# Kernel tuning notes

Hardware: AMD Instinct MI355X
Metric: run time of the kernel (lower is better)

The kernel has to match this reference:

```python
import jax, jax.numpy as jnp
import numpy as np

N, F, H, O = 16384, 64, 128, 512

def setup_inputs() -> dict:
    key = jax.random.key(0)
    ks = jax.random.split(key, 5)
    # PyTorch Linear default init: U(-1/sqrt(fan_in), 1/sqrt(fan_in))
    lim1 = 1.0  # fan_in = 1 for Linear(1, H)
    lim2 = 1.0 / np.sqrt(H)
    x = jax.random.normal(ks[0], (N, F), dtype=jnp.float32)
    W1 = jax.random.uniform(ks[1], (F, H), minval=-lim1, maxval=lim1, dtype=jnp.float32)
    b1 = jax.random.uniform(ks[2], (F, H), minval=-lim1, maxval=lim1, dtype=jnp.float32)
    W2 = jax.random.uniform(ks[3], (F, H, O), minval=-lim2, maxval=lim2, dtype=jnp.float32)
    b2 = jax.random.uniform(ks[4], (F, O), minval=-lim2, maxval=lim2, dtype=jnp.float32)
    return {"x": x, "W1": W1, "b1": b1, "W2": W2, "b2": b2}

def reference(x, W1, b1, W2, b2):
    # Per-feature MLP: h_f = W2_f @ elu(x_f * w1_f + b1_f) + b2_f, summed over f.
    # pre: [N, F, H] = outer-product of each scalar feature with its W1 row
    pre = x[:, :, None] * W1[None, :, :] + b1[None, :, :]
    a = jax.nn.elu(pre)                                  # [N, F, H]
    h = jnp.einsum('nfh,fho->no', a, W2)                 # sum over f and h
    h = h + jnp.sum(b2, axis=0)[None, :]                 # biases summed over F
    return h / jnp.sqrt(jnp.float32(F))
```

## Files before the change

### kernel.cpp

```cpp
#include <hip/hip_runtime.h>
#include <cstdint>

#define NROWS 16384
#define FDIM 64
#define HDIM 128
#define ODIM 512
#define KDIM 8192

#define BM 64
#define BN 256
#define BK 64

typedef short bf16x8 __attribute__((ext_vector_type(8)));
typedef float f32x4 __attribute__((ext_vector_type(4)));
typedef uint32_t u32x4 __attribute__((ext_vector_type(4)));

__device__ __forceinline__ uint16_t rne_bf16(float f) {
  uint32_t u = __builtin_bit_cast(uint32_t, f);
  u += 0x7fffu + ((u >> 16) & 1u);
  return (uint16_t)(u >> 16);
}

__global__ void prep_w2t(const float* __restrict__ W2, uint16_t* __restrict__ W2T) {
  __shared__ float tile[64][65];
  const int k0 = blockIdx.x * 64;
  const int o0 = blockIdx.y * 64;
  const int tx = threadIdx.x;
  const int ty = threadIdx.y;
#pragma unroll
  for (int j = 0; j < 8; ++j)
    tile[ty + 8 * j][tx] = W2[(size_t)(k0 + ty + 8 * j) * ODIM + o0 + tx];
  __syncthreads();
#pragma unroll
  for (int j = 0; j < 8; ++j)
    W2T[(size_t)(o0 + ty + 8 * j) * KDIM + k0 + tx] = rne_bf16(tile[tx][ty + 8 * j]);
}

__global__ void prep_small(const float* __restrict__ W1, const float* __restrict__ b1,
                           const float* __restrict__ b2, uint16_t* __restrict__ w1bf,
                           uint16_t* __restrict__ b1bf, float* __restrict__ b2sum) {
  const int t = blockIdx.x * 256 + threadIdx.x;
  w1bf[t] = rne_bf16(W1[t]);
  b1bf[t] = rne_bf16(b1[t]);
  if (t < ODIM) {
    float s = 0.f;
#pragma unroll
    for (int f = 0; f < FDIM; ++f) s += b2[(size_t)f * ODIM + t];
    b2sum[t] = s;
  }
}

__global__ __launch_bounds__(256, 3) void mlp_gemm(
    const float* __restrict__ x, const uint16_t* __restrict__ w1bf,
    const uint16_t* __restrict__ b1bf, const uint16_t* __restrict__ W2T,
    const float* __restrict__ b2sum, float* __restrict__ out) {
  __shared__ __align__(16) uint16_t As[BM * BK];
  __shared__ __align__(16) uint16_t Bs[BN * BK];

  const int tid = threadIdx.x;
  const int bid = blockIdx.x;
  const int o0 = (bid & 1) * BN;
  const int m0 = (bid >> 1) * BM;

  const int wid = tid >> 6;
  const int lane = tid & 63;
  const int wn = wid * 64;
  const int q = lane >> 4;
  const int r = lane & 15;

  const int ar = tid >> 3;
  const int ac = tid & 7;
  const int brow = lane >> 3;
  const int bcg = (lane & 7) ^ brow;

  f32x4 acc[4][4];
#pragma unroll
  for (int i = 0; i < 4; ++i)
#pragma unroll
    for (int j = 0; j < 4; ++j) acc[i][j] = {0.f, 0.f, 0.f, 0.f};

  for (int f = 0; f < FDIM; ++f) {
    float xv[2];
#pragma unroll
    for (int i = 0; i < 2; ++i)
      xv[i] = x[(size_t)(m0 + i * 32 + ar) * FDIM + f];

#pragma unroll
    for (int half = 0; half < 2; ++half) {
      const int kk = f * 2 + half;
      __syncthreads();

#pragma unroll
      for (int j = 0; j < 8; ++j) {
        const int chunk = wid * 8 + j;
        const uint16_t* gp =
            W2T + (size_t)(o0 + chunk * 8 + brow) * KDIM + kk * BK + bcg * 8;
        uint16_t* lp = &Bs[chunk * 512];
        __builtin_amdgcn_global_load_lds(
            (const __attribute__((address_space(1))) uint32_t*)gp,
            (__attribute__((address_space(3))) uint32_t*)lp, 16, 0, 0);
      }

      const int hoff = half * 64 + ac * 8;
      u32x4 w1d = *(const u32x4*)(w1bf + f * HDIM + hoff);
      u32x4 b1d = *(const u32x4*)(b1bf + f * HDIM + hoff);
      float w1f[8], b1f[8];
#pragma unroll
      for (int p = 0; p < 4; ++p) {
        w1f[2 * p]     = __builtin_bit_cast(float, w1d[p] << 16);
        w1f[2 * p + 1] = __builtin_bit_cast(float, w1d[p] & 0xffff0000u);
        b1f[2 * p]     = __builtin_bit_cast(float, b1d[p] << 16);
        b1f[2 * p + 1] = __builtin_bit_cast(float, b1d[p] & 0xffff0000u);
      }
#pragma unroll
      for (int i = 0; i < 2; ++i) {
        const int m = i * 32 + ar;
        u32x4 ov;
#pragma unroll
        for (int p = 0; p < 4; ++p) {
          float plo = fmaf(xv[i], w1f[2 * p], b1f[2 * p]);
          float phi = fmaf(xv[i], w1f[2 * p + 1], b1f[2 * p + 1]);
          float elo = plo > 0.f ? plo : __expf(plo) - 1.f;
          float ehi = phi > 0.f ? phi : __expf(phi) - 1.f;
          ov[p] = __builtin_amdgcn_perm(__builtin_bit_cast(uint32_t, ehi),
                                        __builtin_bit_cast(uint32_t, elo),
                                        0x07060302u);
        }
        *(u32x4*)&As[m * BK + ((ac ^ (m & 7)) * 8)] = ov;
      }
      __syncthreads();

#pragma unroll
      for (int kc = 0; kc < 2; ++kc) {
        bf16x8 af[4], bfr[4];
        const int cg = kc * 4 + q;
#pragma unroll
        for (int mt = 0; mt < 4; ++mt) {
          const int row = mt * 16 + r;
          af[mt] = *(const bf16x8*)&As[row * BK + ((cg ^ (row & 7)) * 8)];
        }
#pragma unroll
        for (int nt = 0; nt < 4; ++nt) {
          const int row = wn + nt * 16 + r;
          bfr[nt] = *(const bf16x8*)&Bs[row * BK + ((cg ^ (row & 7)) * 8)];
        }
#pragma unroll
        for (int mt = 0; mt < 4; ++mt)
#pragma unroll
          for (int nt = 0; nt < 4; ++nt)
            acc[mt][nt] = __builtin_amdgcn_mfma_f32_16x16x32_bf16(
                af[mt], bfr[nt], acc[mt][nt], 0, 0, 0);
      }
    }
  }

  float bsv[4];
#pragma unroll
  for (int nt = 0; nt < 4; ++nt) bsv[nt] = b2sum[o0 + wn + nt * 16 + r];
#pragma unroll
  for (int mt = 0; mt < 4; ++mt)
#pragma unroll
    for (int nt = 0; nt < 4; ++nt)
#pragma unroll
      for (int v = 0; v < 4; ++v) {
        const int row = m0 + mt * 16 + q * 4 + v;
        const int col = o0 + wn + nt * 16 + r;
        out[(size_t)row * ODIM + col] = (acc[mt][nt][v] + bsv[nt]) * 0.125f;
      }
}

extern "C" void kernel_launch(void* const* d_in, const int* in_sizes, int n_in,
                              void* d_out, int out_size, void* d_ws, size_t ws_size,
                              hipStream_t stream) {
  const float* x  = (const float*)d_in[0];
  const float* W1 = (const float*)d_in[1];
  const float* b1 = (const float*)d_in[2];
  const float* W2 = (const float*)d_in[3];
  const float* b2 = (const float*)d_in[4];
  float* out = (float*)d_out;

  char* ws = (char*)d_ws;
  float*    b2sum = (float*)ws;
  uint16_t* w1bf  = (uint16_t*)(ws + 4096);
  uint16_t* b1bf  = (uint16_t*)(ws + 4096 + 16384);
  uint16_t* W2T   = (uint16_t*)(ws + 65536);

  prep_w2t<<<dim3(KDIM / 64, ODIM / 64), dim3(64, 8), 0, stream>>>(W2, W2T);
  prep_small<<<32, 256, 0, stream>>>(W1, b1, b2, w1bf, b1bf, b2sum);
  mlp_gemm<<<(NROWS / BM) * (ODIM / BN), 256, 0, stream>>>(x, w1bf, b1bf, W2T,
                                                           b2sum, out);
}
```

Measured before the change: 254.8 us.

## Double-buffer LDS, widen tile to full N, and stagger ELU generation across waves

Each block now covers all 512 output columns with 512 threads, so the ELU activation tile for a row block is computed once instead of once per N-half. A and B tiles are double-buffered in LDS with a single barrier per K-step, and the next step's W2 prefetch and A generation overlap the current step's MFMAs. Half the waves generate A before their MFMAs and half after, which spreads the exp/ALU work against matrix work. The cost is about 144KB of LDS per block, allowing only one block per CU. The grid also shrinks to 256 blocks, which lowers occupancy and increases per-block register pressure.

```diff
diff --git a/kernel.cpp b/kernel.cpp
--- a/kernel.cpp
+++ b/kernel.cpp
@@ -6,9 +6,10 @@
 #define HDIM 128
 #define ODIM 512
 #define KDIM 8192
+#define NSTEPS 128
 
 #define BM 64
-#define BN 256
+#define BN 512
 #define BK 64
 
 typedef short bf16x8 __attribute__((ext_vector_type(8)));
@@ -50,17 +51,15 @@
   }
 }
 
-__global__ __launch_bounds__(256, 3) void mlp_gemm(
+__global__ __launch_bounds__(512, 2) void mlp_gemm(
     const float* __restrict__ x, const uint16_t* __restrict__ w1bf,
     const uint16_t* __restrict__ b1bf, const uint16_t* __restrict__ W2T,
     const float* __restrict__ b2sum, float* __restrict__ out) {
-  __shared__ __align__(16) uint16_t As[BM * BK];
-  __shared__ __align__(16) uint16_t Bs[BN * BK];
+  __shared__ __align__(16) uint16_t As[2][BM * BK];
+  __shared__ __align__(16) uint16_t Bs[2][BN * BK];
 
   const int tid = threadIdx.x;
-  const int bid = blockIdx.x;
-  const int o0 = (bid & 1) * BN;
-  const int m0 = (bid >> 1) * BM;
+  const int m0 = blockIdx.x * BM;
 
   const int wid = tid >> 6;
   const int lane = tid & 63;
@@ -79,84 +78,91 @@
 #pragma unroll
     for (int j = 0; j < 4; ++j) acc[i][j] = {0.f, 0.f, 0.f, 0.f};
 
-  for (int f = 0; f < FDIM; ++f) {
-    float xv[2];
+  auto stageB = [&](int step, int buf) {
 #pragma unroll
-    for (int i = 0; i < 2; ++i)
-      xv[i] = x[(size_t)(m0 + i * 32 + ar) * FDIM + f];
+    for (int j = 0; j < 8; ++j) {
+      const int chunk = wid * 8 + j;
+      const uint16_t* gp =
+          W2T + (size_t)(chunk * 8 + brow) * KDIM + step * BK + bcg * 8;
+      uint16_t* lp = &Bs[buf][chunk * 512];
+      __builtin_amdgcn_global_load_lds(
+          (const __attribute__((address_space(1))) uint32_t*)gp,
+          (__attribute__((address_space(3))) uint32_t*)lp, 16, 0, 0);
+    }
+  };
 
+  auto genA = [&](int step, int buf) {
+    const int f = step >> 1;
+    const int half = step & 1;
+    const float xv = x[(size_t)(m0 + ar) * FDIM + f];
+    const int hoff = half * 64 + ac * 8;
+    u32x4 w1d = *(const u32x4*)(w1bf + f * HDIM + hoff);
+    u32x4 b1d = *(const u32x4*)(b1bf + f * HDIM + hoff);
+    u32x4 ov;
 #pragma unroll
-    for (int half = 0; half < 2; ++half) {
-      const int kk = f * 2 + half;
-      __syncthreads();
+    for (int p = 0; p < 4; ++p) {
+      float wlo = __builtin_bit_cast(float, w1d[p] << 16);
+      float whi = __builtin_bit_cast(float, w1d[p] & 0xffff0000u);
+      float blo = __builtin_bit_cast(float, b1d[p] << 16);
+      float bhi = __builtin_bit_cast(float, b1d[p] & 0xffff0000u);
+      float plo = fmaf(xv, wlo, blo);
+      float phi = fmaf(xv, whi, bhi);
+      float elo = plo > 0.f ? plo : __expf(plo) - 1.f;
+      float ehi = phi > 0.f ? phi : __expf(phi) - 1.f;
+      ov[p] = __builtin_amdgcn_perm(__builtin_bit_cast(uint32_t, ehi),
+                                    __builtin_bit_cast(uint32_t, elo),
+                                    0x07060302u);
+    }
+    *(u32x4*)&As[buf][ar * BK + ((ac ^ (ar & 7)) * 8)] = ov;
+  };
 
+  auto domfma = [&](int buf) {
 #pragma unroll
-      for (int j = 0; j < 8; ++j) {
-        const int chunk = wid * 8 + j;
-        const uint16_t* gp =
-            W2T + (size_t)(o0 + chunk * 8 + brow) * KDIM + kk * BK + bcg * 8;
-        uint16_t* lp = &Bs[chunk * 512];
-        __builtin_amdgcn_global_load_lds(
-            (const __attribute__((address_space(1))) uint32_t*)gp,
-            (__attribute__((address_space(3))) uint32_t*)lp, 16, 0, 0);
-      }
-
-      const int hoff = half * 64 + ac * 8;
-      u32x4 w1d = *(const u32x4*)(w1bf + f * HDIM + hoff);
-      u32x4 b1d = *(const u32x4*)(b1bf + f * HDIM + hoff);
-      float w1f[8], b1f[8];
+    for (int kc = 0; kc < 2; ++kc) {
+      bf16x8 af[4], bfr[4];
+      const int cg = kc * 4 + q;
 #pragma unroll
-      for (int p = 0; p < 4; ++p) {
-        w1f[2 * p]     = __builtin_bit_cast(float, w1d[p] << 16);
-        w1f[2 * p + 1] = __builtin_bit_cast(float, w1d[p] & 0xffff0000u);
-        b1f[2 * p]     = __builtin_bit_cast(float, b1d[p] << 16);
-        b1f[2 * p + 1] = __builtin_bit_cast(float, b1d[p] & 0xffff0000u);
+      for (int mt = 0; mt < 4; ++mt) {
+        const int row = mt * 16 + r;
+        af[mt] = *(const bf16x8*)&As[buf][row * BK + ((cg ^ (row & 7)) * 8)];
       }
 #pragma unroll
-      for (int i = 0; i < 2; ++i) {
-        const int m = i * 32 + ar;
-        u32x4 ov;
+      for (int nt = 0; nt < 4; ++nt) {
+        const int row = wn + nt * 16 + r;
+        bfr[nt] = *(const bf16x8*)&Bs[buf][row * BK + ((cg ^ (row & 7)) * 8)];
+      }
 #pragma unroll
-        for (int p = 0; p < 4; ++p) {
-          float plo = fmaf(xv[i], w1f[2 * p], b1f[2 * p]);
-          float phi = fmaf(xv[i], w1f[2 * p + 1], b1f[2 * p + 1]);
-          float elo = plo > 0.f ? plo : __expf(plo) - 1.f;
-          float ehi = phi > 0.f ? phi : __expf(phi) - 1.f;
-          ov[p] = __builtin_amdgcn_perm(__builtin_bit_cast(uint32_t, ehi),
-                                        __builtin_bit_cast(uint32_t, elo),
-                                        0x07060302u);
-        }
-        *(u32x4*)&As[m * BK + ((ac ^ (m & 7)) * 8)] = ov;
+      for (int mt = 0; mt < 4; ++mt)
+#pragma unroll
+        for (int nt = 0; nt < 4; ++nt)
+          acc[mt][nt] = __builtin_amdgcn_mfma_f32_16x16x32_bf16(
+              af[mt], bfr[nt], acc[mt][nt], 0, 0, 0);
+    }
+  };
+
+  stageB(0, 0);
+  genA(0, 0);
+
+  for (int s = 0; s < NSTEPS; ++s) {
+    const int cur = s & 1;
+    const int nxt = cur ^ 1;
+    __syncthreads();
+    if (wid < 4) {
+      if (s + 1 < NSTEPS) {
+        stageB(s + 1, nxt);
+        genA(s + 1, nxt);
       }
-      __syncthreads();
-
-#pragma unroll
-      for (int kc = 0; kc < 2; ++kc) {
-        bf16x8 af[4], bfr[4];
-        const int cg = kc * 4 + q;
-#pragma unroll
-        for (int mt = 0; mt < 4; ++mt) {
-          const int row = mt * 16 + r;
-          af[mt] = *(const bf16x8*)&As[row * BK + ((cg ^ (row & 7)) * 8)];
-        }
-#pragma unroll
-        for (int nt = 0; nt < 4; ++nt) {
-          const int row = wn + nt * 16 + r;
-          bfr[nt] = *(const bf16x8*)&Bs[row * BK + ((cg ^ (row & 7)) * 8)];
-        }
-#pragma unroll
-        for (int mt = 0; mt < 4; ++mt)
-#pragma unroll
-          for (int nt = 0; nt < 4; ++nt)
-            acc[mt][nt] = __builtin_amdgcn_mfma_f32_16x16x32_bf16(
-                af[mt], bfr[nt], acc[mt][nt], 0, 0, 0);
-      }
+      domfma(cur);
+    } else {
+      if (s + 1 < NSTEPS) stageB(s + 1, nxt);
+      domfma(cur);
+      if (s + 1 < NSTEPS) genA(s + 1, nxt);
     }
   }
 
   float bsv[4];
 #pragma unroll
-  for (int nt = 0; nt < 4; ++nt) bsv[nt] = b2sum[o0 + wn + nt * 16 + r];
+  for (int nt = 0; nt < 4; ++nt) bsv[nt] = b2sum[wn + nt * 16 + r];
 #pragma unroll
   for (int mt = 0; mt < 4; ++mt)
 #pragma unroll
@@ -164,7 +170,7 @@
 #pragma unroll
       for (int v = 0; v < 4; ++v) {
         const int row = m0 + mt * 16 + q * 4 + v;
-        const int col = o0 + wn + nt * 16 + r;
+        const int col = wn + nt * 16 + r;
         out[(size_t)row * ODIM + col] = (acc[mt][nt][v] + bsv[nt]) * 0.125f;
       }
 }
@@ -187,6 +193,5 @@
 
   prep_w2t<<<dim3(KDIM / 64, ODIM / 64), dim3(64, 8), 0, stream>>>(W2, W2T);
   prep_small<<<32, 256, 0, stream>>>(W1, b1, b2, w1bf, b1bf, b2sum);
-  mlp_gemm<<<(NROWS / BM) * (ODIM / BN), 256, 0, stream>>>(x, w1bf, b1bf, W2T,
-                                                           b2sum, out);
+  mlp_gemm<<<NROWS / BM, 512, 0, stream>>>(x, w1bf, b1bf, W2T, b2sum, out);
 }
```

Result: slower. 298.9 us (+17.3%).

## Double GEMM M-tile and split K in two with atomic accumulation

Applied to the files above, without the earlier changes.

The M tile grows from 64 to 128 rows, so each wave computes a 64x128 sub-tile and each staged W2 tile is reused across twice as many rows. To keep the grid at 512 blocks, the K dimension (feature axis) is split in half across blocks, and partial results are combined with float atomic adds into an output that a memset zeroes first. This reduces W2 traffic per output and raises MFMA density per LDS load. In exchange it adds the memset, atomic write traffic, and higher register pressure (launch bounds drop to 2 blocks per SM), and the summation order is no longer deterministic.

```diff
diff --git a/kernel.cpp b/kernel.cpp
--- a/kernel.cpp
+++ b/kernel.cpp
@@ -6,8 +6,9 @@
 #define HDIM 128
 #define ODIM 512
 #define KDIM 8192
+#define NSTEPS 64
 
-#define BM 64
+#define BM 128
 #define BN 256
 #define BK 64
 
@@ -50,7 +51,7 @@
   }
 }
 
-__global__ __launch_bounds__(256, 3) void mlp_gemm(
+__global__ __launch_bounds__(256, 2) void mlp_gemm(
     const float* __restrict__ x, const uint16_t* __restrict__ w1bf,
     const uint16_t* __restrict__ b1bf, const uint16_t* __restrict__ W2T,
     const float* __restrict__ b2sum, float* __restrict__ out) {
@@ -59,114 +60,108 @@
 
   const int tid = threadIdx.x;
   const int bid = blockIdx.x;
-  const int o0 = (bid & 1) * BN;
-  const int m0 = (bid >> 1) * BM;
+  const int oh = bid & 1;
+  const int kh = (bid >> 1) & 1;
+  const int m0 = (bid >> 2) * BM;
+  const int o0 = oh * BN;
 
   const int wid = tid >> 6;
   const int lane = tid & 63;
-  const int wn = wid * 64;
+  const int mh = wid >> 1;
+  const int nh = wid & 1;
   const int q = lane >> 4;
   const int r = lane & 15;
 
-  const int ar = tid >> 3;
-  const int ac = tid & 7;
+  const int arow = tid >> 1;
+  const int gbase = (tid & 1) * 4;
   const int brow = lane >> 3;
   const int bcg = (lane & 7) ^ brow;
 
-  f32x4 acc[4][4];
+  f32x4 acc[4][8];
 #pragma unroll
   for (int i = 0; i < 4; ++i)
 #pragma unroll
-    for (int j = 0; j < 4; ++j) acc[i][j] = {0.f, 0.f, 0.f, 0.f};
+    for (int j = 0; j < 8; ++j) acc[i][j] = {0.f, 0.f, 0.f, 0.f};
 
-  for (int f = 0; f < FDIM; ++f) {
-    float xv[2];
-#pragma unroll
-    for (int i = 0; i < 2; ++i)
-      xv[i] = x[(size_t)(m0 + i * 32 + ar) * FDIM + f];
+  for (int s = 0; s < NSTEPS; ++s) {
+    const int kstep = kh * 64 + s;
+    __syncthreads();
 
 #pragma unroll
-    for (int half = 0; half < 2; ++half) {
-      const int kk = f * 2 + half;
-      __syncthreads();
+    for (int j = 0; j < 8; ++j) {
+      const int chunk = wid * 8 + j;
+      const uint16_t* gp =
+          W2T + (size_t)(o0 + chunk * 8 + brow) * KDIM + kstep * BK + bcg * 8;
+      uint16_t* lp = &Bs[chunk * 512];
+      __builtin_amdgcn_global_load_lds(
+          (const __attribute__((address_space(1))) uint32_t*)gp,
+          (__attribute__((address_space(3))) uint32_t*)lp, 16, 0, 0);
+    }
 
+    {
+      const int f = kh * 32 + (s >> 1);
+      const int half = s & 1;
+      const float xv = x[(size_t)(m0 + arow) * FDIM + f];
 #pragma unroll
-      for (int j = 0; j < 8; ++j) {
-        const int chunk = wid * 8 + j;
-        const uint16_t* gp =
-            W2T + (size_t)(o0 + chunk * 8 + brow) * KDIM + kk * BK + bcg * 8;
-        uint16_t* lp = &Bs[chunk * 512];
-        __builtin_amdgcn_global_load_lds(
-            (const __attribute__((address_space(1))) uint32_t*)gp,
-            (__attribute__((address_space(3))) uint32_t*)lp, 16, 0, 0);
-      }
-
-      const int hoff = half * 64 + ac * 8;
-      u32x4 w1d = *(const u32x4*)(w1bf + f * HDIM + hoff);
-      u32x4 b1d = *(const u32x4*)(b1bf + f * HDIM + hoff);
-      float w1f[8], b1f[8];
-#pragma unroll
-      for (int p = 0; p < 4; ++p) {
-        w1f[2 * p]     = __builtin_bit_cast(float, w1d[p] << 16);
-        w1f[2 * p + 1] = __builtin_bit_cast(float, w1d[p] & 0xffff0000u);
-        b1f[2 * p]     = __builtin_bit_cast(float, b1d[p] << 16);
-        b1f[2 * p + 1] = __builtin_bit_cast(float, b1d[p] & 0xffff0000u);
-      }
-#pragma unroll
-      for (int i = 0; i < 2; ++i) {
-        const int m = i * 32 + ar;
+      for (int gi = 0; gi < 4; ++gi) {
+        const int g = gbase + gi;
+        const int hoff = half * 64 + g * 8;
+        u32x4 w1d = *(const u32x4*)(w1bf + f * HDIM + hoff);
+        u32x4 b1d = *(const u32x4*)(b1bf + f * HDIM + hoff);
         u32x4 ov;
 #pragma unroll
         for (int p = 0; p < 4; ++p) {
-          float plo = fmaf(xv[i], w1f[2 * p], b1f[2 * p]);
-          float phi = fmaf(xv[i], w1f[2 * p + 1], b1f[2 * p + 1]);
+          float wlo = __builtin_bit_cast(float, w1d[p] << 16);
+          float whi = __builtin_bit_cast(float, w1d[p] & 0xffff0000u);
+          float blo = __builtin_bit_cast(float, b1d[p] << 16);
+          float bhi = __builtin_bit_cast(float, b1d[p] & 0xffff0000u);
+          float plo = fmaf(xv, wlo, blo);
+          float phi = fmaf(xv, whi, bhi);
           float elo = plo > 0.f ? plo : __expf(plo) - 1.f;
           float ehi = phi > 0.f ? phi : __expf(phi) - 1.f;
           ov[p] = __builtin_amdgcn_perm(__builtin_bit_cast(uint32_t, ehi),
                                         __builtin_bit_cast(uint32_t, elo),
                                         0x07060302u);
         }
-        *(u32x4*)&As[m * BK + ((ac ^ (m & 7)) * 8)] = ov;
+        *(u32x4*)&As[arow * BK + ((g ^ (arow & 7)) * 8)] = ov;
       }
-      __syncthreads();
+    }
+    __syncthreads();
 
 #pragma unroll
-      for (int kc = 0; kc < 2; ++kc) {
-        bf16x8 af[4], bfr[4];
-        const int cg = kc * 4 + q;
+    for (int kc = 0; kc < 2; ++kc) {
+      const int cg = kc * 4 + q;
+      bf16x8 af[4];
 #pragma unroll
-        for (int mt = 0; mt < 4; ++mt) {
-          const int row = mt * 16 + r;
-          af[mt] = *(const bf16x8*)&As[row * BK + ((cg ^ (row & 7)) * 8)];
-        }
+      for (int mt = 0; mt < 4; ++mt) {
+        const int row = mh * 64 + mt * 16 + r;
+        af[mt] = *(const bf16x8*)&As[row * BK + ((cg ^ (row & 7)) * 8)];
+      }
 #pragma unroll
-        for (int nt = 0; nt < 4; ++nt) {
-          const int row = wn + nt * 16 + r;
-          bfr[nt] = *(const bf16x8*)&Bs[row * BK + ((cg ^ (row & 7)) * 8)];
-        }
+      for (int nt = 0; nt < 8; ++nt) {
+        const int row = nh * 128 + nt * 16 + r;
+        bf16x8 bf = *(const bf16x8*)&Bs[row * BK + ((cg ^ (row & 7)) * 8)];
 #pragma unroll
         for (int mt = 0; mt < 4; ++mt)
-#pragma unroll
-          for (int nt = 0; nt < 4; ++nt)
-            acc[mt][nt] = __builtin_amdgcn_mfma_f32_16x16x32_bf16(
-                af[mt], bfr[nt], acc[mt][nt], 0, 0, 0);
+          acc[mt][nt] = __builtin_amdgcn_mfma_f32_16x16x32_bf16(
+              af[mt], bf, acc[mt][nt], 0, 0, 0);
       }
     }
   }
 
-  float bsv[4];
 #pragma unroll
-  for (int nt = 0; nt < 4; ++nt) bsv[nt] = b2sum[o0 + wn + nt * 16 + r];
+  for (int nt = 0; nt < 8; ++nt) {
+    const int col = o0 + nh * 128 + nt * 16 + r;
+    const float bias = (kh == 0) ? b2sum[col] * 0.125f : 0.f;
 #pragma unroll
-  for (int mt = 0; mt < 4; ++mt)
-#pragma unroll
-    for (int nt = 0; nt < 4; ++nt)
+    for (int mt = 0; mt < 4; ++mt)
 #pragma unroll
       for (int v = 0; v < 4; ++v) {
-        const int row = m0 + mt * 16 + q * 4 + v;
-        const int col = o0 + wn + nt * 16 + r;
-        out[(size_t)row * ODIM + col] = (acc[mt][nt][v] + bsv[nt]) * 0.125f;
+        const int row = m0 + mh * 64 + mt * 16 + q * 4 + v;
+        unsafeAtomicAdd(&out[(size_t)row * ODIM + col],
+                        acc[mt][nt][v] * 0.125f + bias);
       }
+  }
 }
 
 extern "C" void kernel_launch(void* const* d_in, const int* in_sizes, int n_in,
@@ -185,8 +180,8 @@
   uint16_t* b1bf  = (uint16_t*)(ws + 4096 + 16384);
   uint16_t* W2T   = (uint16_t*)(ws + 65536);
 
+  hipMemsetAsync(out, 0, (size_t)NROWS * ODIM * sizeof(float), stream);
   prep_w2t<<<dim3(KDIM / 64, ODIM / 64), dim3(64, 8), 0, stream>>>(W2, W2T);
   prep_small<<<32, 256, 0, stream>>>(W1, b1, b2, w1bf, b1bf, b2sum);
-  mlp_gemm<<<(NROWS / BM) * (ODIM / BN), 256, 0, stream>>>(x, w1bf, b1bf, W2T,
-                                                           b2sum, out);
+  mlp_gemm<<<512, 256, 0, stream>>>(x, w1bf, b1bf, W2T, b2sum, out);
 }
```

Result: slower. 288.1 us (+13.1%).
